# Optimization experiments

Measured on AMD Instinct MI355X. Metric: run time of the kernel, lower is better.

## Reference

```python
import jax, jax.numpy as jnp
import numpy as np

N = 4096     # batch of positions
E = 32       # descriptor buckets (experts)
NBLK = 12    # residual blocks per head


def _ln(x, g, b, eps=1e-5):
    m = x.mean(-1, keepdims=True)
    v = ((x - m) ** 2).mean(-1, keepdims=True)
    return (x - m) / jnp.sqrt(v + eps) * g + b


def _gelu(x):
    return jax.nn.gelu(x, approximate=False)  # torch nn.GELU default = exact erf


def setup_inputs() -> dict:
    key = jax.random.key(0)
    ks = iter(jax.random.split(key, 64))

    def nrm(shape, scale=0.05):
        return jax.random.normal(next(ks), shape, jnp.float32) * scale

    return {
        "piece_idx": jax.random.randint(next(ks), (N, 64), 0, 12),
        "side_flag": jax.random.randint(next(ks), (N,), 0, 2),
        "ep_file": jax.random.randint(next(ks), (N,), 0, 8),
        "castle_ms": jax.random.uniform(next(ks), (N, 4), jnp.float32),
        "fifty_a": jax.random.uniform(next(ks), (N,), jnp.float32),
        "descriptor_index": jax.random.randint(next(ks), (N,), 0, E),
        # per-bucket embedding tables, stacked on a leading expert axis
        "Wp_w": nrm((E, 64, 12, 32)), "Wp_b": nrm((E, 64, 12, 32)),
        "Wc_w": nrm((E, 4, 32)), "Wc_b": nrm((E, 4, 32)),
        "Wep_w": nrm((E, 8, 32)), "Wep_b": nrm((E, 8, 32)),
        "Wf_w": nrm((E, 2, 32)), "Wf_b": nrm((E, 2, 32)),
        # per-bucket MLP head params (weights stored as [in,out])
        "fc1_w": nrm((E, 2240, 256)), "fc1_b": nrm((E, 256)),
        "ln1_g": jnp.ones((E, 256)), "ln1_b": jnp.zeros((E, 256)),
        "fc2_w": nrm((E, 256, 32)), "fc2_b": nrm((E, 32)),
        "ln2_g": jnp.ones((E, 32)), "ln2_b": jnp.zeros((E, 32)),
        "blkA_w": nrm((NBLK, E, 32, 32)), "blkA_b": nrm((NBLK, E, 32)),
        "blkA_g": jnp.ones((NBLK, E, 32)), "blkA_be": jnp.zeros((NBLK, E, 32)),
        "blkB_w": nrm((NBLK, E, 32, 32)), "blkB_b": nrm((NBLK, E, 32)),
        "blkB_g": jnp.ones((NBLK, E, 32)), "blkB_be": jnp.zeros((NBLK, E, 32)),
        "out_w": nrm((E, 32, 51)), "out_b": nrm((E, 51)),
        "bins": jnp.linspace(0.0, 1.0, 51),
    }


def reference(piece_idx, side_flag, ep_file, castle_ms, fifty_a, descriptor_index,
              Wp_w, Wp_b, Wc_w, Wc_b, Wep_w, Wep_b, Wf_w, Wf_b,
              fc1_w, fc1_b, ln1_g, ln1_b, fc2_w, fc2_b, ln2_g, ln2_b,
              blkA_w, blkA_b, blkA_g, blkA_be, blkB_w, blkB_b, blkB_g, blkB_be,
              out_w, out_b, bins):
    desc = descriptor_index
    side = side_flag.astype(bool)
    n = piece_idx.shape[0]

    # ---- per-bucket, side-selected embedding gathers -> x_emb [N,2240] ----
    sq = jnp.arange(64)
    pc = jnp.maximum(piece_idx, 0)                                 # clamp -1 -> 0
    w_emb = Wp_w[desc[:, None], sq[None, :], pc]                    # [N,64,32]
    b_emb = Wp_b[desc[:, None], sq[None, :], pc]
    piece_emb = jnp.where(side[:, None, None], b_emb, w_emb)
    piece_emb = piece_emb * (piece_idx >= 0)[..., None].astype(piece_emb.dtype)
    pieces_vec = piece_emb.reshape(n, 2048)

    Wc = jnp.where(side[:, None, None], Wc_b[desc], Wc_w[desc])     # [N,4,32]
    castle_vec = (castle_ms[..., None] * Wc).reshape(n, 128)

    Wep = jnp.where(side[:, None, None], Wep_b[desc], Wep_w[desc])  # [N,8,32]
    epc = jnp.maximum(ep_file, 0)
    ep_vec = jnp.take_along_axis(Wep, epc[:, None, None], axis=1)[:, 0]
    ep_vec = ep_vec * (ep_file >= 0)[:, None].astype(ep_vec.dtype)

    Wf = jnp.where(side[:, None, None], Wf_b[desc], Wf_w[desc])     # [N,2,32]
    fifty_vec = (1.0 - fifty_a)[:, None] * Wf[:, 0] + fifty_a[:, None] * Wf[:, 1]

    x = jnp.concatenate([pieces_vec, castle_vec, ep_vec, fifty_vec], axis=1)  # [N,2240]

    # ---- expert-routed dense layer: all-expert GEMM + per-token select ----
    def dense_moe(h, W, b):
        ha = jnp.einsum('nd,edh->neh', h, W)                        # [N,E,out]
        hsel = jnp.take_along_axis(ha, desc[:, None, None], axis=1)[:, 0]
        return hsel + b[desc]

    h = _ln(_gelu(dense_moe(x, fc1_w, fc1_b)), ln1_g[desc], ln1_b[desc])   # [N,256]
    h = _ln(_gelu(dense_moe(h, fc2_w, fc2_b)), ln2_g[desc], ln2_b[desc])   # [N,32]

    def blk(carry, p):
        wA, bA, gA, beA, wB, bB, gB, beB = p
        y = _ln(_gelu(dense_moe(carry, wA, bA)), gA[desc], beA[desc])
        y = _ln(_gelu(dense_moe(y, wB, bB)), gB[desc], beB[desc])
        return carry + y, None

    h, _ = jax.lax.scan(blk, h, (blkA_w, blkA_b, blkA_g, blkA_be,
                                 blkB_w, blkB_b, blkB_g, blkB_be))

    logits = dense_moe(_gelu(h), out_w, out_b)                      # [N,51]
    p_win = jnp.sum(jax.nn.softmax(logits, axis=-1) * bins, axis=-1, keepdims=True)
    return logits, p_win
```

## Files before the change

### kernel.cpp

```cpp
#include <hip/hip_runtime.h>
#include <math.h>

#define N 4096
#define E 32
#define NBLK 12
#define D_IN 2240
#define H1 256
#define H2 32
#define NOUT 51
#define MT 16
#define NPAD (N + E*(MT-1))
#define NTILE (NPAD/MT)
#define KSPLIT 4
#define NROWS 4608
#define GMAX 96
#define NCONVBLK (35*4*E)

typedef short s8v __attribute__((ext_vector_type(8)));
typedef float f4v __attribute__((ext_vector_type(4)));

__device__ __forceinline__ float gelu(float x){
    return 0.5f * x * (1.0f + erff(x * 0.70710678118654752f));
}
__device__ __forceinline__ unsigned short f2bf(float f){
    unsigned int u = __float_as_uint(f);
    unsigned int r = (u + 0x7fffu + ((u >> 16) & 1u)) >> 16;
    return (unsigned short)r;
}
__device__ __forceinline__ float bflo(unsigned int u){ return __uint_as_float(u << 16); }
__device__ __forceinline__ float bfhi(unsigned int u){ return __uint_as_float(u & 0xffff0000u); }

__global__ void k_sort(const int* __restrict__ desc,
                       int* __restrict__ perm, int* __restrict__ tile_e,
                       int4* __restrict__ garr, int* __restrict__ ngroups){
    __shared__ int scnt[E];
    __shared__ int spoff[E+1];
    __shared__ int scur[E];
    int tid = threadIdx.x;
    if (tid < E) scnt[tid] = 0;
    __syncthreads();
    for (int n = tid; n < N; n += blockDim.x) atomicAdd(&scnt[desc[n]], 1);
    __syncthreads();
    if (tid == 0){
        int run = 0;
        for (int e = 0; e < E; e++){ spoff[e] = run; run += ((scnt[e] + MT - 1)/MT)*MT; }
        spoff[E] = run;
        int ng = 0;
        for (int e = 0; e < E; e++){
            int t0 = spoff[e]/MT, t1 = spoff[e+1]/MT;
            for (int t = t0; t < t1; t += 8){
                int nv = t1 - t; if (nv > 8) nv = 8;
                if (ng < GMAX) garr[ng] = make_int4(t, e, nv, 0);
                ng++;
            }
        }
        *ngroups = (ng > GMAX) ? GMAX : ng;
    }
    __syncthreads();
    if (tid < E) scur[tid] = spoff[tid];
    for (int p = tid; p < NPAD; p += blockDim.x) perm[p] = -1;
    __syncthreads();
    for (int n = tid; n < N; n += blockDim.x){
        int p = atomicAdd(&scur[desc[n]], 1);
        perm[p] = n;
    }
    for (int t = tid; t < NTILE; t += blockDim.x){
        int p0 = t*MT;
        int e = -1;
        if (p0 < spoff[E]){
            for (int q = 0; q < E; q++){
                if (p0 >= spoff[q] && p0 < spoff[q+1]){ e = q; break; }
            }
        }
        tile_e[t] = e;
    }
}

__global__ void k_prep(const int* __restrict__ perm,
                       const int* __restrict__ piece_idx,
                       const int* __restrict__ side_flag,
                       const int* __restrict__ ep_file,
                       const float* __restrict__ castle_ms,
                       const float* __restrict__ fifty_a,
                       const int* __restrict__ desc_idx,
                       const float* __restrict__ Wp_w, const float* __restrict__ Wp_b,
                       const float* __restrict__ Wc_w, const float* __restrict__ Wc_b,
                       const float* __restrict__ Wep_w, const float* __restrict__ Wep_b,
                       const float* __restrict__ Wf_w, const float* __restrict__ Wf_b,
                       unsigned short* __restrict__ xs,
                       const float* __restrict__ W1, unsigned short* __restrict__ Wt){
    __shared__ float lds[64][65];
    int tid = threadIdx.x;
    if (blockIdx.x >= NPAD){
        int b = blockIdx.x - NPAD;
        int kt = b % 35;
        int nt = (b / 35) & 3;
        int e  = b / 140;
        int k0 = kt*64, n0 = nt*64;
        int kk = tid >> 4, nn = (tid & 15) * 4;
        const float* src = W1 + ((size_t)e*D_IN + k0)*H1 + n0;
        #pragma unroll
        for (int r = 0; r < 4; r++){
            float4 v = *(const float4*)(src + (size_t)(kk + r*16)*H1 + nn);
            lds[kk + r*16][nn]   = v.x;
            lds[kk + r*16][nn+1] = v.y;
            lds[kk + r*16][nn+2] = v.z;
            lds[kk + r*16][nn+3] = v.w;
        }
        __syncthreads();
        int n = tid >> 2, kq = tid & 3;
        s8v p0, p1;
        #pragma unroll
        for (int j = 0; j < 8; j++) p0[j] = (short)f2bf(lds[kq*16 + j][n]);
        #pragma unroll
        for (int j = 0; j < 8; j++) p1[j] = (short)f2bf(lds[kq*16 + 8 + j][n]);
        unsigned short* dst = Wt + ((size_t)(e*H1 + n0 + n))*D_IN + k0 + kq*16;
        *(s8v*)dst       = p0;
        *(s8v*)(dst + 8) = p1;
        return;
    }
    int pos = blockIdx.x;
    int row = perm[pos];
    unsigned short* xr = xs + (size_t)pos * D_IN;
    if (row < 0){
        s8v z = {0,0,0,0,0,0,0,0};
        for (int t = tid; t < D_IN/8; t += blockDim.x) *(s8v*)(xr + t*8) = z;
        return;
    }
    int d = desc_idx[row];
    int s = side_flag[row];
    __shared__ int pidx[64];
    if (tid < 64) pidx[tid] = piece_idx[row*64 + tid];
    __syncthreads();
    const float* Wp  = s ? Wp_b  : Wp_w;
    const float* Wc  = s ? Wc_b  : Wc_w;
    const float* Wep = s ? Wep_b : Wep_w;
    const float* Wf  = s ? Wf_b  : Wf_w;
    int ep  = ep_file[row];
    int epc = ep > 0 ? ep : 0;
    float a = fifty_a[row];
    for (int t = tid; t < D_IN/8; t += blockDim.x){
        int i0 = t*8;
        float v[8];
        if (i0 < 2048){
            int sq = i0 >> 5, c0 = i0 & 31;
            int pc = pidx[sq];
            float msk = pc >= 0 ? 1.0f : 0.0f;
            int pcc = pc > 0 ? pc : 0;
            const float* base = Wp + (((size_t)d*64 + sq)*12 + pcc)*32 + c0;
            float4 a0 = *(const float4*)base;
            float4 a1 = *(const float4*)(base + 4);
            v[0]=a0.x*msk; v[1]=a0.y*msk; v[2]=a0.z*msk; v[3]=a0.w*msk;
            v[4]=a1.x*msk; v[5]=a1.y*msk; v[6]=a1.z*msk; v[7]=a1.w*msk;
        } else if (i0 < 2176){
            int j = i0 - 2048; int ci = j >> 5, c0 = j & 31;
            float cv = castle_ms[row*4 + ci];
            const float* base = Wc + ((size_t)d*4 + ci)*32 + c0;
            float4 a0 = *(const float4*)base;
            float4 a1 = *(const float4*)(base + 4);
            v[0]=a0.x*cv; v[1]=a0.y*cv; v[2]=a0.z*cv; v[3]=a0.w*cv;
            v[4]=a1.x*cv; v[5]=a1.y*cv; v[6]=a1.z*cv; v[7]=a1.w*cv;
        } else if (i0 < 2208){
            int c0 = i0 - 2176;
            float msk = ep >= 0 ? 1.0f : 0.0f;
            const float* base = Wep + ((size_t)d*8 + epc)*32 + c0;
            float4 a0 = *(const float4*)base;
            float4 a1 = *(const float4*)(base + 4);
            v[0]=a0.x*msk; v[1]=a0.y*msk; v[2]=a0.z*msk; v[3]=a0.w*msk;
            v[4]=a1.x*msk; v[5]=a1.y*msk; v[6]=a1.z*msk; v[7]=a1.w*msk;
        } else {
            int c0 = i0 - 2208;
            #pragma unroll
            for (int j = 0; j < 8; j++)
                v[j] = (1.0f - a) * Wf[(size_t)d*64 + c0 + j] + a * Wf[(size_t)d*64 + 32 + c0 + j];
        }
        s8v p;
        #pragma unroll
        for (int j = 0; j < 8; j++) p[j] = (short)f2bf(v[j]);
        *(s8v*)(xr + i0) = p;
    }
}

__launch_bounds__(256)
__global__ void k_fc1(const int4* __restrict__ garr, const int* __restrict__ ngroups,
                      const unsigned short* __restrict__ xs,
                      const unsigned short* __restrict__ Wt,
                      float* __restrict__ h1p){
    int g = blockIdx.x;
    if (g >= *ngroups) return;
    int4 gi = garr[g];
    int tile0 = gi.x, e = gi.y, nv = gi.z;
    int kc = blockIdx.y, nh = blockIdx.z;
    int kstart = (kc <= 2) ? kc*18 : 53;
    int nsteps = (kc < 2) ? 18 : 17;
    int lane = threadIdx.x & 63, wave = threadIdx.x >> 6;
    int quad = lane >> 4, l16 = lane & 15;
    int col0 = nh*128 + wave*32 + l16;
    const unsigned short* Ab = xs + (size_t)(tile0*MT + l16)*D_IN + quad*8;
    const unsigned short* B0 = Wt + ((size_t)e*H1 + col0)*D_IN + quad*8;
    const unsigned short* B1 = B0 + (size_t)16*D_IN;
    f4v acc[8][2];
    #pragma unroll
    for (int mt = 0; mt < 8; mt++){ acc[mt][0] = (f4v){0.f,0.f,0.f,0.f}; acc[mt][1] = (f4v){0.f,0.f,0.f,0.f}; }
    int kend = kstart + nsteps;
    #pragma unroll 2
    for (int s = kstart; s < kend; s++){
        int ko = s*32;
        s8v b0 = *(const s8v*)(B0 + ko);
        s8v b1 = *(const s8v*)(B1 + ko);
        #pragma unroll
        for (int mt = 0; mt < 8; mt++){
            s8v av = *(const s8v*)(Ab + (size_t)mt*MT*D_IN + ko);
            acc[mt][0] = __builtin_amdgcn_mfma_f32_16x16x32_bf16(av, b0, acc[mt][0], 0, 0, 0);
            acc[mt][1] = __builtin_amdgcn_mfma_f32_16x16x32_bf16(av, b1, acc[mt][1], 0, 0, 0);
        }
    }
    float* out = h1p + (size_t)kc*NROWS*H1;
    #pragma unroll
    for (int mt = 0; mt < 8; mt++){
        if (mt >= nv) break;
        int posb = (tile0 + mt)*MT + quad*4;
        #pragma unroll
        for (int r = 0; r < 4; r++){
            out[(size_t)(posb + r)*H1 + col0]      = acc[mt][0][r];
            out[(size_t)(posb + r)*H1 + col0 + 16] = acc[mt][1][r];
        }
    }
}

__launch_bounds__(512)
__global__ void k_tail(const int* __restrict__ tile_e, const int* __restrict__ perm,
                       const float* __restrict__ h1p, const float* __restrict__ b1,
                       const float* __restrict__ g1, const float* __restrict__ be1,
                       const float* __restrict__ W2, const float* __restrict__ b2,
                       const float* __restrict__ g2, const float* __restrict__ be2,
                       const float* __restrict__ Aw, const float* __restrict__ Abv,
                       const float* __restrict__ Ag, const float* __restrict__ Abe,
                       const float* __restrict__ Bw, const float* __restrict__ Bb,
                       const float* __restrict__ Bg, const float* __restrict__ Bbe,
                       const float* __restrict__ Ow, const float* __restrict__ Ob,
                       const float* __restrict__ bins,
                       float* __restrict__ out){
    int t = blockIdx.x;
    int e = tile_e[t];
    if (e < 0) return;
    int tid = threadIdx.x;

    __shared__ __align__(16) unsigned int smem[12288];
    __shared__ __align__(16) float vecs[NBLK*6*32];
    __shared__ __align__(16) float sh2[MT][36];
    __shared__ __align__(16) float sh3[MT][36];

    float* shf = (float*)smem;
    unsigned int* W2pk = smem + 4160;

    {
        const float* W2e = W2 + (size_t)e*H1*H2;
        for (int j = tid; j < 4096; j += 512){
            int h = j & 1, q = j >> 1, cc = q & 31, p2 = q >> 5;
            int k0 = 4*p2 + 2*h;
            unsigned int lo = f2bf(W2e[k0*32 + cc]);
            unsigned int hi = f2bf(W2e[(k0+1)*32 + cc]);
            W2pk[(p2*32 + cc)*2 + h] = lo | (hi << 16);
        }
    }
    for (int j = tid; j < NBLK*6*32; j += 512){
        int cc = j & 31, vi = (j >> 5) % 6, tb = j / 192;
        size_t wb = (size_t)tb*E + e;
        const float* src;
        switch(vi){ case 0: src=Abv; break; case 1: src=Ag; break; case 2: src=Abe; break;
                    case 3: src=Bb;  break; case 4: src=Bg; break; default: src=Bbe; }
        vecs[j] = src[wb*32 + cc];
    }
    for (int slot = tid; slot < MT*64; slot += 512){
        int r = slot >> 6, c4 = (slot & 63) << 2;
        int row = t*MT + r;
        float4 v = {0.f,0.f,0.f,0.f};
        #pragma unroll
        for (int kc = 0; kc < KSPLIT; kc++){
            float4 p = *(const float4*)(h1p + ((size_t)kc*NROWS + row)*H1 + c4);
            v.x += p.x; v.y += p.y; v.z += p.z; v.w += p.w;
        }
        float4 bb = *(const float4*)(b1 + e*H1 + c4);
        float4 g4;
        g4.x = gelu(v.x + bb.x); g4.y = gelu(v.y + bb.y);
        g4.z = gelu(v.z + bb.z); g4.w = gelu(v.w + bb.w);
        *(float4*)(shf + r*260 + c4) = g4;
    }
    __syncthreads();

    int m = tid >> 5, c = tid & 31;
    {
        float s = 0.f;
        #pragma unroll
        for (int j = 0; j < 8; j++) s += shf[m*260 + c + 32*j];
        #pragma unroll
        for (int o = 16; o > 0; o >>= 1) s += __shfl_xor(s, o);
        float mean = s * (1.0f/H1);
        float v2 = 0.f;
        #pragma unroll
        for (int j = 0; j < 8; j++){ float d = shf[m*260 + c + 32*j] - mean; v2 += d*d; }
        #pragma unroll
        for (int o = 16; o > 0; o >>= 1) v2 += __shfl_xor(v2, o);
        float rs = rsqrtf(v2 * (1.0f/H1) + 1e-5f);
        #pragma unroll
        for (int j = 0; j < 8; j++){
            int k = c + 32*j;
            shf[m*260 + k] = (shf[m*260 + k] - mean) * rs * g1[e*H1 + k] + be1[e*H1 + k];
        }
    }
    float hv;
    {
        const uint2* W2p = (const uint2*)W2pk;
        float q0=0.f,q1=0.f,q2=0.f,q3=0.f;
        #pragma unroll 8
        for (int p2 = 0; p2 < 64; p2++){
            uint2 w = W2p[p2*32 + c];
            float4 h4 = *(const float4*)(shf + m*260 + p2*4);
            q0 = fmaf(h4.x, bflo(w.x), q0);
            q1 = fmaf(h4.y, bfhi(w.x), q1);
            q2 = fmaf(h4.z, bflo(w.y), q2);
            q3 = fmaf(h4.w, bfhi(w.y), q3);
        }
        float acc = (q0+q1) + (q2+q3) + b2[e*H2 + c];
        float y = gelu(acc);
        float ss = y;
        #pragma unroll
        for (int o = 16; o > 0; o >>= 1) ss += __shfl_xor(ss, o);
        float mean2 = ss * (1.0f/H2);
        float dv = y - mean2;
        float vv = dv*dv;
        #pragma unroll
        for (int o = 16; o > 0; o >>= 1) vv += __shfl_xor(vv, o);
        hv = dv * rsqrtf(vv*(1.0f/H2) + 1e-5f) * g2[e*H2+c] + be2[e*H2+c];
    }
    __syncthreads();

    for (int j = tid; j < 12288; j += 512){
        int tbsub = j >> 9, r = j & 511;
        int h = r & 1, q = r >> 1, cc = q & 31, p2 = q >> 5;
        int k0 = 4*p2 + 2*h;
        const float* src = (tbsub & 1) ? Bw : Aw;
        size_t base = ((size_t)(tbsub >> 1)*E + e)*1024;
        unsigned int lo = f2bf(src[base + k0*32 + cc]);
        unsigned int hi = f2bf(src[base + (k0+1)*32 + cc]);
        smem[j] = lo | (hi << 16);
    }
    __syncthreads();

    for (int tb = 0; tb < NBLK; tb++){
        const float* vA = &vecs[tb*192];
        const uint2* WA = (const uint2*)(smem + (tb*2+0)*512);
        const uint2* WB = (const uint2*)(smem + (tb*2+1)*512);
        sh2[m][c] = hv;
        float q0=0.f,q1=0.f,q2=0.f,q3=0.f;
        #pragma unroll
        for (int p2 = 0; p2 < 8; p2++){
            uint2 w = WA[p2*32 + c];
            float4 h4 = *(const float4*)(&sh2[m][p2*4]);
            q0 = fmaf(h4.x, bflo(w.x), q0);
            q1 = fmaf(h4.y, bfhi(w.x), q1);
            q2 = fmaf(h4.z, bflo(w.y), q2);
            q3 = fmaf(h4.w, bfhi(w.y), q3);
        }
        float ya = (q0+q1) + (q2+q3) + vA[c];
        ya = gelu(ya);
        float sa = ya;
        #pragma unroll
        for (int o = 16; o > 0; o >>= 1) sa += __shfl_xor(sa, o);
        float ma = sa * (1.0f/H2);
        float da = ya - ma;
        float va = da*da;
        #pragma unroll
        for (int o = 16; o > 0; o >>= 1) va += __shfl_xor(va, o);
        float yA = da * rsqrtf(va*(1.0f/H2) + 1e-5f) * vA[32+c] + vA[64+c];
        sh3[m][c] = yA;
        q0=0.f; q1=0.f; q2=0.f; q3=0.f;
        #pragma unroll
        for (int p2 = 0; p2 < 8; p2++){
            uint2 w = WB[p2*32 + c];
            float4 h4 = *(const float4*)(&sh3[m][p2*4]);
            q0 = fmaf(h4.x, bflo(w.x), q0);
            q1 = fmaf(h4.y, bfhi(w.x), q1);
            q2 = fmaf(h4.z, bflo(w.y), q2);
            q3 = fmaf(h4.w, bfhi(w.y), q3);
        }
        float yb = (q0+q1) + (q2+q3) + vA[96+c];
        yb = gelu(yb);
        float sb2 = yb;
        #pragma unroll
        for (int o = 16; o > 0; o >>= 1) sb2 += __shfl_xor(sb2, o);
        float mb = sb2 * (1.0f/H2);
        float db = yb - mb;
        float vb = db*db;
        #pragma unroll
        for (int o = 16; o > 0; o >>= 1) vb += __shfl_xor(vb, o);
        hv += db * rsqrtf(vb*(1.0f/H2) + 1e-5f) * vA[128+c] + vA[160+c];
    }

    sh2[m][c] = gelu(hv);
    __syncthreads();
    int wave = tid >> 6, lane = tid & 63;
    const float* W = Ow + (size_t)e*32*NOUT;
    for (int rr = wave; rr < MT; rr += 8){
        int orow = perm[t*MT + rr];
        if (orow < 0) continue;
        float acc = (lane < NOUT) ? Ob[e*NOUT + lane] : -INFINITY;
        #pragma unroll
        for (int k = 0; k < 32; k++){
            float gk = sh2[rr][k];
            if (lane < NOUT) acc = fmaf(gk, W[k*NOUT + lane], acc);
        }
        if (lane < NOUT) out[(size_t)orow*NOUT + lane] = acc;
        float mx = acc;
        #pragma unroll
        for (int o = 32; o > 0; o >>= 1) mx = fmaxf(mx, __shfl_xor(mx, o));
        float pp = (lane < NOUT) ? expf(acc - mx) : 0.0f;
        float sum = pp;
        #pragma unroll
        for (int o = 32; o > 0; o >>= 1) sum += __shfl_xor(sum, o);
        float pb = (lane < NOUT) ? pp * bins[lane] : 0.0f;
        float sb = pb;
        #pragma unroll
        for (int o = 32; o > 0; o >>= 1) sb += __shfl_xor(sb, o);
        if (lane == 0) out[(size_t)N*NOUT + orow] = sb / sum;
    }
}

extern "C" void kernel_launch(void* const* d_in, const int* in_sizes, int n_in,
                              void* d_out, int out_size, void* d_ws, size_t ws_size,
                              hipStream_t stream){
    const int*   piece_idx = (const int*)d_in[0];
    const int*   side_flag = (const int*)d_in[1];
    const int*   ep_file   = (const int*)d_in[2];
    const float* castle_ms = (const float*)d_in[3];
    const float* fifty_a   = (const float*)d_in[4];
    const int*   desc      = (const int*)d_in[5];
    const float* Wp_w  = (const float*)d_in[6];
    const float* Wp_b  = (const float*)d_in[7];
    const float* Wc_w  = (const float*)d_in[8];
    const float* Wc_b  = (const float*)d_in[9];
    const float* Wep_w = (const float*)d_in[10];
    const float* Wep_b = (const float*)d_in[11];
    const float* Wf_w  = (const float*)d_in[12];
    const float* Wf_b  = (const float*)d_in[13];
    const float* fc1_w = (const float*)d_in[14];
    const float* fc1_b = (const float*)d_in[15];
    const float* ln1_g = (const float*)d_in[16];
    const float* ln1_b = (const float*)d_in[17];
    const float* fc2_w = (const float*)d_in[18];
    const float* fc2_b = (const float*)d_in[19];
    const float* ln2_g = (const float*)d_in[20];
    const float* ln2_b = (const float*)d_in[21];
    const float* blkA_w  = (const float*)d_in[22];
    const float* blkA_b  = (const float*)d_in[23];
    const float* blkA_g  = (const float*)d_in[24];
    const float* blkA_be = (const float*)d_in[25];
    const float* blkB_w  = (const float*)d_in[26];
    const float* blkB_b  = (const float*)d_in[27];
    const float* blkB_g  = (const float*)d_in[28];
    const float* blkB_be = (const float*)d_in[29];
    const float* out_w = (const float*)d_in[30];
    const float* out_b = (const float*)d_in[31];
    const float* bins  = (const float*)d_in[32];

    char* wsp = (char*)d_ws;
    auto alloc = [&](size_t bytes){ void* p = (void*)wsp; wsp += (bytes + 255) & ~(size_t)255; return p; };
    int*            perm    = (int*)            alloc((size_t)NPAD*4);
    int*            tile_e  = (int*)            alloc((size_t)NTILE*4);
    int4*           garr    = (int4*)           alloc((size_t)GMAX*16);
    int*            ngroups = (int*)            alloc(256);
    unsigned short* Wt      = (unsigned short*) alloc((size_t)E*H1*D_IN*2);
    unsigned short* xs      = (unsigned short*) alloc((size_t)(NPAD+128)*D_IN*2);
    float*          h1p     = (float*)          alloc((size_t)KSPLIT*NROWS*H1*4);

    k_sort<<<1, 256, 0, stream>>>(desc, perm, tile_e, garr, ngroups);
    k_prep<<<NPAD + NCONVBLK, 256, 0, stream>>>(perm, piece_idx, side_flag, ep_file,
                                                castle_ms, fifty_a, desc,
                                                Wp_w, Wp_b, Wc_w, Wc_b,
                                                Wep_w, Wep_b, Wf_w, Wf_b,
                                                xs, fc1_w, Wt);
    k_fc1<<<dim3(GMAX, KSPLIT, 2), 256, 0, stream>>>(garr, ngroups, xs, Wt, h1p);
    k_tail<<<NTILE, 512, 0, stream>>>(tile_e, perm, h1p, fc1_b, ln1_g, ln1_b,
                                      fc2_w, fc2_b, ln2_g, ln2_b,
                                      blkA_w, blkA_b, blkA_g, blkA_be,
                                      blkB_w, blkB_b, blkB_g, blkB_be,
                                      out_w, out_b, bins, (float*)d_out);
}
```

Baseline: 312.2 us.

## Fuse fc1 GEMM into per-tile tail kernel, drop split-K partial buffer

Removes the separate grouped split-K fc1 kernel and its fp32 partial-sum workspace. Each 16-row tile block now stages its bf16 activations in LDS and computes the full 256-column fc1 output with MFMA before continuing into the existing tail. This saves a launch and the write-then-reread of four partial buffers. In exchange, each tile block streams the full expert weight slice itself, with no weight reuse across up to 8 tiles, and the GEMM runs on only ~290 blocks.

```diff
diff --git a/kernel.cpp b/kernel.cpp
--- a/kernel.cpp
+++ b/kernel.cpp
@@ -11,10 +11,8 @@
 #define MT 16
 #define NPAD (N + E*(MT-1))
 #define NTILE (NPAD/MT)
-#define KSPLIT 4
-#define NROWS 4608
-#define GMAX 96
 #define NCONVBLK (35*4*E)
+#define APITCH 1128
 
 typedef short s8v __attribute__((ext_vector_type(8)));
 typedef float f4v __attribute__((ext_vector_type(4)));
@@ -31,8 +29,7 @@
 __device__ __forceinline__ float bfhi(unsigned int u){ return __uint_as_float(u & 0xffff0000u); }
 
 __global__ void k_sort(const int* __restrict__ desc,
-                       int* __restrict__ perm, int* __restrict__ tile_e,
-                       int4* __restrict__ garr, int* __restrict__ ngroups){
+                       int* __restrict__ perm, int* __restrict__ tile_e){
     __shared__ int scnt[E];
     __shared__ int spoff[E+1];
     __shared__ int scur[E];
@@ -45,16 +42,6 @@
         int run = 0;
         for (int e = 0; e < E; e++){ spoff[e] = run; run += ((scnt[e] + MT - 1)/MT)*MT; }
         spoff[E] = run;
-        int ng = 0;
-        for (int e = 0; e < E; e++){
-            int t0 = spoff[e]/MT, t1 = spoff[e+1]/MT;
-            for (int t = t0; t < t1; t += 8){
-                int nv = t1 - t; if (nv > 8) nv = 8;
-                if (ng < GMAX) garr[ng] = make_int4(t, e, nv, 0);
-                ng++;
-            }
-        }
-        *ngroups = (ng > GMAX) ? GMAX : ng;
     }
     __syncthreads();
     if (tid < E) scur[tid] = spoff[tid];
@@ -181,56 +168,11 @@
     }
 }
 
-__launch_bounds__(256)
-__global__ void k_fc1(const int4* __restrict__ garr, const int* __restrict__ ngroups,
-                      const unsigned short* __restrict__ xs,
-                      const unsigned short* __restrict__ Wt,
-                      float* __restrict__ h1p){
-    int g = blockIdx.x;
-    if (g >= *ngroups) return;
-    int4 gi = garr[g];
-    int tile0 = gi.x, e = gi.y, nv = gi.z;
-    int kc = blockIdx.y, nh = blockIdx.z;
-    int kstart = (kc <= 2) ? kc*18 : 53;
-    int nsteps = (kc < 2) ? 18 : 17;
-    int lane = threadIdx.x & 63, wave = threadIdx.x >> 6;
-    int quad = lane >> 4, l16 = lane & 15;
-    int col0 = nh*128 + wave*32 + l16;
-    const unsigned short* Ab = xs + (size_t)(tile0*MT + l16)*D_IN + quad*8;
-    const unsigned short* B0 = Wt + ((size_t)e*H1 + col0)*D_IN + quad*8;
-    const unsigned short* B1 = B0 + (size_t)16*D_IN;
-    f4v acc[8][2];
-    #pragma unroll
-    for (int mt = 0; mt < 8; mt++){ acc[mt][0] = (f4v){0.f,0.f,0.f,0.f}; acc[mt][1] = (f4v){0.f,0.f,0.f,0.f}; }
-    int kend = kstart + nsteps;
-    #pragma unroll 2
-    for (int s = kstart; s < kend; s++){
-        int ko = s*32;
-        s8v b0 = *(const s8v*)(B0 + ko);
-        s8v b1 = *(const s8v*)(B1 + ko);
-        #pragma unroll
-        for (int mt = 0; mt < 8; mt++){
-            s8v av = *(const s8v*)(Ab + (size_t)mt*MT*D_IN + ko);
-            acc[mt][0] = __builtin_amdgcn_mfma_f32_16x16x32_bf16(av, b0, acc[mt][0], 0, 0, 0);
-            acc[mt][1] = __builtin_amdgcn_mfma_f32_16x16x32_bf16(av, b1, acc[mt][1], 0, 0, 0);
-        }
-    }
-    float* out = h1p + (size_t)kc*NROWS*H1;
-    #pragma unroll
-    for (int mt = 0; mt < 8; mt++){
-        if (mt >= nv) break;
-        int posb = (tile0 + mt)*MT + quad*4;
-        #pragma unroll
-        for (int r = 0; r < 4; r++){
-            out[(size_t)(posb + r)*H1 + col0]      = acc[mt][0][r];
-            out[(size_t)(posb + r)*H1 + col0 + 16] = acc[mt][1][r];
-        }
-    }
-}
-
 __launch_bounds__(512)
-__global__ void k_tail(const int* __restrict__ tile_e, const int* __restrict__ perm,
-                       const float* __restrict__ h1p, const float* __restrict__ b1,
+__global__ void k_main(const int* __restrict__ tile_e, const int* __restrict__ perm,
+                       const unsigned short* __restrict__ xs,
+                       const unsigned short* __restrict__ Wt,
+                       const float* __restrict__ b1,
                        const float* __restrict__ g1, const float* __restrict__ be1,
                        const float* __restrict__ W2, const float* __restrict__ b2,
                        const float* __restrict__ g2, const float* __restrict__ be2,
@@ -245,15 +187,63 @@
     int e = tile_e[t];
     if (e < 0) return;
     int tid = threadIdx.x;
+    int wave = tid >> 6, lane = tid & 63;
+    int quad = lane >> 4, l16 = lane & 15;
 
     __shared__ __align__(16) unsigned int smem[12288];
     __shared__ __align__(16) float vecs[NBLK*6*32];
     __shared__ __align__(16) float sh2[MT][36];
     __shared__ __align__(16) float sh3[MT][36];
 
+    for (int j = tid; j < NBLK*6*32; j += 512){
+        int cc = j & 31, vi = (j >> 5) % 6, tb = j / 192;
+        size_t wb = (size_t)tb*E + e;
+        const float* src;
+        switch(vi){ case 0: src=Abv; break; case 1: src=Ag; break; case 2: src=Abe; break;
+                    case 3: src=Bb;  break; case 4: src=Bg; break; default: src=Bbe; }
+        vecs[j] = src[wb*32 + cc];
+    }
+
+    int col0 = wave*32 + l16;
+    const unsigned short* B0g = Wt + ((size_t)e*H1 + col0)*D_IN + quad*8;
+    const unsigned short* B1g = B0g + (size_t)16*D_IN;
+    unsigned short* As = (unsigned short*)smem;
+    f4v acc0 = {0.f,0.f,0.f,0.f}, acc1 = {0.f,0.f,0.f,0.f};
+    #pragma unroll
+    for (int kh = 0; kh < 2; kh++){
+        __syncthreads();
+        for (int q = tid; q < 2240; q += 512){
+            int r = q / 140, jj = (q % 140) * 8;
+            s8v v = *(const s8v*)(xs + (size_t)(t*MT + r)*D_IN + kh*1120 + jj);
+            *(s8v*)(As + r*APITCH + jj) = v;
+        }
+        __syncthreads();
+        const unsigned short* Arow = As + l16*APITCH + quad*8;
+        #pragma unroll 5
+        for (int s = 0; s < 35; s++){
+            int kg = kh*35 + s;
+            s8v av = *(const s8v*)(Arow + s*32);
+            s8v b0 = *(const s8v*)(B0g + kg*32);
+            s8v b1v= *(const s8v*)(B1g + kg*32);
+            acc0 = __builtin_amdgcn_mfma_f32_16x16x32_bf16(av, b0, acc0, 0, 0, 0);
+            acc1 = __builtin_amdgcn_mfma_f32_16x16x32_bf16(av, b1v, acc1, 0, 0, 0);
+        }
+    }
+    __syncthreads();
+
     float* shf = (float*)smem;
     unsigned int* W2pk = smem + 4160;
 
+    {
+        float bb0 = b1[e*H1 + col0];
+        float bb1 = b1[e*H1 + col0 + 16];
+        #pragma unroll
+        for (int r = 0; r < 4; r++){
+            int row = quad*4 + r;
+            shf[row*260 + col0]      = gelu(acc0[r] + bb0);
+            shf[row*260 + col0 + 16] = gelu(acc1[r] + bb1);
+        }
+    }
     {
         const float* W2e = W2 + (size_t)e*H1*H2;
         for (int j = tid; j < 4096; j += 512){
@@ -263,29 +253,6 @@
             unsigned int hi = f2bf(W2e[(k0+1)*32 + cc]);
             W2pk[(p2*32 + cc)*2 + h] = lo | (hi << 16);
         }
-    }
-    for (int j = tid; j < NBLK*6*32; j += 512){
-        int cc = j & 31, vi = (j >> 5) % 6, tb = j / 192;
-        size_t wb = (size_t)tb*E + e;
-        const float* src;
-        switch(vi){ case 0: src=Abv; break; case 1: src=Ag; break; case 2: src=Abe; break;
-                    case 3: src=Bb;  break; case 4: src=Bg; break; default: src=Bbe; }
-        vecs[j] = src[wb*32 + cc];
-    }
-    for (int slot = tid; slot < MT*64; slot += 512){
-        int r = slot >> 6, c4 = (slot & 63) << 2;
-        int row = t*MT + r;
-        float4 v = {0.f,0.f,0.f,0.f};
-        #pragma unroll
-        for (int kc = 0; kc < KSPLIT; kc++){
-            float4 p = *(const float4*)(h1p + ((size_t)kc*NROWS + row)*H1 + c4);
-            v.x += p.x; v.y += p.y; v.z += p.z; v.w += p.w;
-        }
-        float4 bb = *(const float4*)(b1 + e*H1 + c4);
-        float4 g4;
-        g4.x = gelu(v.x + bb.x); g4.y = gelu(v.y + bb.y);
-        g4.z = gelu(v.z + bb.z); g4.w = gelu(v.w + bb.w);
-        *(float4*)(shf + r*260 + c4) = g4;
     }
     __syncthreads();
 
@@ -338,7 +305,8 @@
 
     for (int j = tid; j < 12288; j += 512){
         int tbsub = j >> 9, r = j & 511;
-        int h = r & 1, q = r >> 1, cc = q & 31, p2 = q >> 5;
+        int h = r & 1, q = r >> 1, cc = q & 31, p2 = q >> 1 >> 4;
+        p2 = (r >> 1) >> 5;
         int k0 = 4*p2 + 2*h;
         const float* src = (tbsub & 1) ? Bw : Aw;
         size_t base = ((size_t)(tbsub >> 1)*E + e)*1024;
@@ -400,7 +368,6 @@
 
     sh2[m][c] = gelu(hv);
     __syncthreads();
-    int wave = tid >> 6, lane = tid & 63;
     const float* W = Ow + (size_t)e*32*NOUT;
     for (int rr = wave; rr < MT; rr += 8){
         int orow = perm[t*MT + rr];
@@ -468,20 +435,16 @@
     auto alloc = [&](size_t bytes){ void* p = (void*)wsp; wsp += (bytes + 255) & ~(size_t)255; return p; };
     int*            perm    = (int*)            alloc((size_t)NPAD*4);
     int*            tile_e  = (int*)            alloc((size_t)NTILE*4);
-    int4*           garr    = (int4*)           alloc((size_t)GMAX*16);
-    int*            ngroups = (int*)            alloc(256);
     unsigned short* Wt      = (unsigned short*) alloc((size_t)E*H1*D_IN*2);
     unsigned short* xs      = (unsigned short*) alloc((size_t)(NPAD+128)*D_IN*2);
-    float*          h1p     = (float*)          alloc((size_t)KSPLIT*NROWS*H1*4);
-
-    k_sort<<<1, 256, 0, stream>>>(desc, perm, tile_e, garr, ngroups);
+
+    k_sort<<<1, 256, 0, stream>>>(desc, perm, tile_e);
     k_prep<<<NPAD + NCONVBLK, 256, 0, stream>>>(perm, piece_idx, side_flag, ep_file,
                                                 castle_ms, fifty_a, desc,
                                                 Wp_w, Wp_b, Wc_w, Wc_b,
                                                 Wep_w, Wep_b, Wf_w, Wf_b,
                                                 xs, fc1_w, Wt);
-    k_fc1<<<dim3(GMAX, KSPLIT, 2), 256, 0, stream>>>(garr, ngroups, xs, Wt, h1p);
-    k_tail<<<NTILE, 512, 0, stream>>>(tile_e, perm, h1p, fc1_b, ln1_g, ln1_b,
+    k_main<<<NTILE, 512, 0, stream>>>(tile_e, perm, xs, Wt, fc1_b, ln1_g, ln1_b,
                                       fc2_w, fc2_b, ln2_g, ln2_b,
                                       blkA_w, blkA_b, blkA_g, blkA_be,
                                       blkB_w, blkB_b, blkB_g, blkB_be,
```

Result: slower. 326.0 us (+4.4%).

## Double tail block to 1024 threads, one wave per row with split-K halves

Applied to the files above, without the earlier changes.

The tail kernel now launches 1024 threads per tile, so each 64-lane wave owns one row. The two half-waves split the K dimension of the fc2 and residual-block matvecs and combine their partial sums with a cross-half shuffle. LayerNorm over 256 is now done with float4 loads and full-wave reductions, and the output head runs one row per wave without the final barrier. This roughly halves the serial per-thread work on the 12-block chain, at the cost of larger blocks, extra shuffles, and possibly lower occupancy or register limits at 1024 threads.

```diff
diff --git a/kernel.cpp b/kernel.cpp
--- a/kernel.cpp
+++ b/kernel.cpp
@@ -228,7 +228,7 @@
     }
 }
 
-__launch_bounds__(512)
+__launch_bounds__(1024)
 __global__ void k_tail(const int* __restrict__ tile_e, const int* __restrict__ perm,
                        const float* __restrict__ h1p, const float* __restrict__ b1,
                        const float* __restrict__ g1, const float* __restrict__ be1,
@@ -245,6 +245,9 @@
     int e = tile_e[t];
     if (e < 0) return;
     int tid = threadIdx.x;
+    int wave = tid >> 6, lane = tid & 63;
+    int c = lane & 31, kk = lane >> 5;
+    int m = wave;
 
     __shared__ __align__(16) unsigned int smem[12288];
     __shared__ __align__(16) float vecs[NBLK*6*32];
@@ -256,7 +259,7 @@
 
     {
         const float* W2e = W2 + (size_t)e*H1*H2;
-        for (int j = tid; j < 4096; j += 512){
+        for (int j = tid; j < 4096; j += 1024){
             int h = j & 1, q = j >> 1, cc = q & 31, p2 = q >> 5;
             int k0 = 4*p2 + 2*h;
             unsigned int lo = f2bf(W2e[k0*32 + cc]);
@@ -264,7 +267,7 @@
             W2pk[(p2*32 + cc)*2 + h] = lo | (hi << 16);
         }
     }
-    for (int j = tid; j < NBLK*6*32; j += 512){
+    for (int j = tid; j < NBLK*6*32; j += 1024){
         int cc = j & 31, vi = (j >> 5) % 6, tb = j / 192;
         size_t wb = (size_t)tb*E + e;
         const float* src;
@@ -272,8 +275,8 @@
                     case 3: src=Bb;  break; case 4: src=Bg; break; default: src=Bbe; }
         vecs[j] = src[wb*32 + cc];
     }
-    for (int slot = tid; slot < MT*64; slot += 512){
-        int r = slot >> 6, c4 = (slot & 63) << 2;
+    {
+        int r = tid >> 6, c4 = (tid & 63) << 2;
         int row = t*MT + r;
         float4 v = {0.f,0.f,0.f,0.f};
         #pragma unroll
@@ -289,32 +292,31 @@
     }
     __syncthreads();
 
-    int m = tid >> 5, c = tid & 31;
     {
-        float s = 0.f;
-        #pragma unroll
-        for (int j = 0; j < 8; j++) s += shf[m*260 + c + 32*j];
-        #pragma unroll
-        for (int o = 16; o > 0; o >>= 1) s += __shfl_xor(s, o);
+        float4 h4 = *(const float4*)(shf + m*260 + lane*4);
+        float s = (h4.x + h4.y) + (h4.z + h4.w);
+        #pragma unroll
+        for (int o = 32; o > 0; o >>= 1) s += __shfl_xor(s, o);
         float mean = s * (1.0f/H1);
-        float v2 = 0.f;
-        #pragma unroll
-        for (int j = 0; j < 8; j++){ float d = shf[m*260 + c + 32*j] - mean; v2 += d*d; }
-        #pragma unroll
-        for (int o = 16; o > 0; o >>= 1) v2 += __shfl_xor(v2, o);
+        float d0 = h4.x-mean, d1 = h4.y-mean, d2 = h4.z-mean, d3 = h4.w-mean;
+        float v2 = (d0*d0 + d1*d1) + (d2*d2 + d3*d3);
+        #pragma unroll
+        for (int o = 32; o > 0; o >>= 1) v2 += __shfl_xor(v2, o);
         float rs = rsqrtf(v2 * (1.0f/H1) + 1e-5f);
-        #pragma unroll
-        for (int j = 0; j < 8; j++){
-            int k = c + 32*j;
-            shf[m*260 + k] = (shf[m*260 + k] - mean) * rs * g1[e*H1 + k] + be1[e*H1 + k];
-        }
+        float4 gg = *(const float4*)(g1 + e*H1 + lane*4);
+        float4 gb = *(const float4*)(be1 + e*H1 + lane*4);
+        float4 hn;
+        hn.x = d0*rs*gg.x + gb.x; hn.y = d1*rs*gg.y + gb.y;
+        hn.z = d2*rs*gg.z + gb.z; hn.w = d3*rs*gg.w + gb.w;
+        *(float4*)(shf + m*260 + lane*4) = hn;
     }
     float hv;
     {
         const uint2* W2p = (const uint2*)W2pk;
         float q0=0.f,q1=0.f,q2=0.f,q3=0.f;
         #pragma unroll 8
-        for (int p2 = 0; p2 < 64; p2++){
+        for (int j = 0; j < 32; j++){
+            int p2 = kk*32 + j;
             uint2 w = W2p[p2*32 + c];
             float4 h4 = *(const float4*)(shf + m*260 + p2*4);
             q0 = fmaf(h4.x, bflo(w.x), q0);
@@ -322,7 +324,9 @@
             q2 = fmaf(h4.z, bflo(w.y), q2);
             q3 = fmaf(h4.w, bfhi(w.y), q3);
         }
-        float acc = (q0+q1) + (q2+q3) + b2[e*H2 + c];
+        float acc = (q0+q1) + (q2+q3);
+        acc += __shfl_xor(acc, 32);
+        acc += b2[e*H2 + c];
         float y = gelu(acc);
         float ss = y;
         #pragma unroll
@@ -336,9 +340,10 @@
     }
     __syncthreads();
 
-    for (int j = tid; j < 12288; j += 512){
+    for (int j = tid; j < 12288; j += 1024){
         int tbsub = j >> 9, r = j & 511;
-        int h = r & 1, q = r >> 1, cc = q & 31, p2 = q >> 5;
+        int h = r & 1, q = r >> 1, cc = q & 31;
+        int p2 = q >> 5;
         int k0 = 4*p2 + 2*h;
         const float* src = (tbsub & 1) ? Bw : Aw;
         size_t base = ((size_t)(tbsub >> 1)*E + e)*1024;
@@ -355,7 +360,8 @@
         sh2[m][c] = hv;
         float q0=0.f,q1=0.f,q2=0.f,q3=0.f;
         #pragma unroll
-        for (int p2 = 0; p2 < 8; p2++){
+        for (int j = 0; j < 4; j++){
+            int p2 = kk*4 + j;
             uint2 w = WA[p2*32 + c];
             float4 h4 = *(const float4*)(&sh2[m][p2*4]);
             q0 = fmaf(h4.x, bflo(w.x), q0);
@@ -363,7 +369,9 @@
             q2 = fmaf(h4.z, bflo(w.y), q2);
             q3 = fmaf(h4.w, bfhi(w.y), q3);
         }
-        float ya = (q0+q1) + (q2+q3) + vA[c];
+        float ya = (q0+q1) + (q2+q3);
+        ya += __shfl_xor(ya, 32);
+        ya += vA[c];
         ya = gelu(ya);
         float sa = ya;
         #pragma unroll
@@ -377,7 +385,8 @@
         sh3[m][c] = yA;
         q0=0.f; q1=0.f; q2=0.f; q3=0.f;
         #pragma unroll
-        for (int p2 = 0; p2 < 8; p2++){
+        for (int j = 0; j < 4; j++){
+            int p2 = kk*4 + j;
             uint2 w = WB[p2*32 + c];
             float4 h4 = *(const float4*)(&sh3[m][p2*4]);
             q0 = fmaf(h4.x, bflo(w.x), q0);
@@ -385,7 +394,9 @@
             q2 = fmaf(h4.z, bflo(w.y), q2);
             q3 = fmaf(h4.w, bfhi(w.y), q3);
         }
-        float yb = (q0+q1) + (q2+q3) + vA[96+c];
+        float yb = (q0+q1) + (q2+q3);
+        yb += __shfl_xor(yb, 32);
+        yb += vA[96+c];
         yb = gelu(yb);
         float sb2 = yb;
         #pragma unroll
@@ -399,32 +410,28 @@
     }
 
     sh2[m][c] = gelu(hv);
-    __syncthreads();
-    int wave = tid >> 6, lane = tid & 63;
+    int orow = perm[t*MT + m];
+    if (orow < 0) return;
     const float* W = Ow + (size_t)e*32*NOUT;
-    for (int rr = wave; rr < MT; rr += 8){
-        int orow = perm[t*MT + rr];
-        if (orow < 0) continue;
-        float acc = (lane < NOUT) ? Ob[e*NOUT + lane] : -INFINITY;
-        #pragma unroll
-        for (int k = 0; k < 32; k++){
-            float gk = sh2[rr][k];
-            if (lane < NOUT) acc = fmaf(gk, W[k*NOUT + lane], acc);
-        }
-        if (lane < NOUT) out[(size_t)orow*NOUT + lane] = acc;
-        float mx = acc;
-        #pragma unroll
-        for (int o = 32; o > 0; o >>= 1) mx = fmaxf(mx, __shfl_xor(mx, o));
-        float pp = (lane < NOUT) ? expf(acc - mx) : 0.0f;
-        float sum = pp;
-        #pragma unroll
-        for (int o = 32; o > 0; o >>= 1) sum += __shfl_xor(sum, o);
-        float pb = (lane < NOUT) ? pp * bins[lane] : 0.0f;
-        float sb = pb;
-        #pragma unroll
-        for (int o = 32; o > 0; o >>= 1) sb += __shfl_xor(sb, o);
-        if (lane == 0) out[(size_t)N*NOUT + orow] = sb / sum;
-    }
+    float acc = (lane < NOUT) ? Ob[e*NOUT + lane] : -INFINITY;
+    #pragma unroll
+    for (int k = 0; k < 32; k++){
+        float gk = sh2[m][k];
+        if (lane < NOUT) acc = fmaf(gk, W[k*NOUT + lane], acc);
+    }
+    if (lane < NOUT) out[(size_t)orow*NOUT + lane] = acc;
+    float mx = acc;
+    #pragma unroll
+    for (int o = 32; o > 0; o >>= 1) mx = fmaxf(mx, __shfl_xor(mx, o));
+    float pp = (lane < NOUT) ? expf(acc - mx) : 0.0f;
+    float sum = pp;
+    #pragma unroll
+    for (int o = 32; o > 0; o >>= 1) sum += __shfl_xor(sum, o);
+    float pb = (lane < NOUT) ? pp * bins[lane] : 0.0f;
+    float sb = pb;
+    #pragma unroll
+    for (int o = 32; o > 0; o >>= 1) sb += __shfl_xor(sb, o);
+    if (lane == 0) out[(size_t)N*NOUT + orow] = sb / sum;
 }
 
 extern "C" void kernel_launch(void* const* d_in, const int* in_sizes, int n_in,
@@ -481,9 +488,9 @@
                                                 Wep_w, Wep_b, Wf_w, Wf_b,
                                                 xs, fc1_w, Wt);
     k_fc1<<<dim3(GMAX, KSPLIT, 2), 256, 0, stream>>>(garr, ngroups, xs, Wt, h1p);
-    k_tail<<<NTILE, 512, 0, stream>>>(tile_e, perm, h1p, fc1_b, ln1_g, ln1_b,
-                                      fc2_w, fc2_b, ln2_g, ln2_b,
-                                      blkA_w, blkA_b, blkA_g, blkA_be,
-                                      blkB_w, blkB_b, blkB_g, blkB_be,
-                                      out_w, out_b, bins, (float*)d_out);
-}
+    k_tail<<<NTILE, 1024, 0, stream>>>(tile_e, perm, h1p, fc1_b, ln1_g, ln1_b,
+                                       fc2_w, fc2_b, ln2_g, ln2_b,
+                                       blkA_w, blkA_b, blkA_g, blkA_be,
+                                       blkB_w, blkB_b, blkB_g, blkB_be,
+                                       out_w, out_b, bins, (float*)d_out);
+}
```

Result: slower. 340.5 us (+9.0%).
